# Kernel optimization log

Hardware: AMD Instinct MI355X
Metric: run time of the kernel (lower is better)

Reference implementation:

```python
import jax, jax.numpy as jnp
import numpy as np

B, C, F, NCLS, NWAY = 512, 1024, 14, 100, 64


def setup_inputs() -> dict:
    key = jax.random.key(0)
    k1, k2, k3 = jax.random.split(key, 3)
    query_features = jax.random.normal(k1, (B, C, F, F), dtype=jnp.float32)
    labels = jax.random.randint(k2, (B,), 0, NWAY)
    prototypes = jax.random.normal(k3, (NCLS, C), dtype=jnp.float32) * 0.05
    indices = jnp.arange(NWAY)  # inverse class mapping: episode class i -> global row
    return {"query_features": query_features, "labels": labels,
            "prototypes": prototypes, "indices": indices, "n_way": NWAY}


def reference(query_features, labels, prototypes, indices, n_way):
    b, c, h, w = query_features.shape
    fsq = h * w
    protos = prototypes[indices]                      # [n_way, C]
    # [B,C,H,W] -> [B*H*W, C], matching permute(0,2,3,1).reshape
    q = jnp.transpose(query_features, (0, 2, 3, 1)).reshape(-1, c)
    # -||q - p||^2 via GEMM trick (same math as expanded pairwise diff)
    qn = jnp.sum(q * q, axis=1, keepdims=True)        # [N,1]
    pn = jnp.sum(protos * protos, axis=1)             # [n_way]
    logits = -(qn + pn[None, :] - 2.0 * (q @ protos.T))  # [N, n_way]
    expanded_labels = jnp.repeat(labels, fsq)         # each pixel inherits image label
    logp = jax.nn.log_softmax(logits, axis=1)
    loss = -jnp.mean(jnp.take_along_axis(logp, expanded_labels[:, None], axis=1))
    return loss
```

## Files before the change

kernel.cpp:

```cpp
#include <hip/hip_runtime.h>
#include <hip/hip_bf16.h>

#define C_DIM 1024
#define HW    196
#define NWAY  64
#define HALF_M 98
#define M_PAD 112
#define MT    7
#define BK    64
#define LDK   72
#define N_TOT (512 * 196)

typedef short bf16x8 __attribute__((ext_vector_type(8)));
typedef float floatx4 __attribute__((ext_vector_type(4)));

__device__ __forceinline__ unsigned short f2bf(float x) {
    unsigned int u = __float_as_uint(x);
    u += 0x7fffu + ((u >> 16) & 1u);
    return (unsigned short)(u >> 16);
}

__device__ __forceinline__ bf16x8 pack8(const float v[8]) {
    bf16x8 r;
#pragma unroll
    for (int i = 0; i < 8; ++i) r[i] = (short)f2bf(v[i]);
    return r;
}

__global__ __launch_bounds__(256) void dfmn_main(
    const float* __restrict__ qf, const int* __restrict__ labels,
    const float* __restrict__ protos, const int* __restrict__ indices,
    float* __restrict__ out)
{
    __shared__ __align__(16) float smem[6370];
    __shared__ float pn_lds[NWAY];
    __shared__ float wsum[4];

    const int t    = threadIdx.x;
    const int lane = t & 63;
    const int wave = t >> 6;

    const int x    = blockIdx.x;
    const int xcd  = x & 7;
    const int grp  = x >> 3;
    const int half = grp & 1;
    const int b    = (grp >> 1) * 8 + xcd;
    const int hw0  = half * HALF_M;

    unsigned short* a_lds = (unsigned short*)smem;
    unsigned short* b_lds = a_lds + M_PAD * LDK;
    float* logits = smem;

    {
        const int cls = t >> 2, part = t & 3;
        const int gid = indices[cls];
        const float4* prow = (const float4*)(protos + (size_t)gid * C_DIM) + part * 64;
        float s = 0.f;
#pragma unroll 4
        for (int i = 0; i < 64; ++i) {
            float4 v = prow[i];
            s += v.x * v.x + v.y * v.y + v.z * v.z + v.w * v.w;
        }
        smem[t] = s;
    }
    __syncthreads();
    if (t < NWAY) pn_lds[t] = smem[4 * t] + smem[4 * t + 1] + smem[4 * t + 2] + smem[4 * t + 3];
    __syncthreads();

    const int boct = t & 7;
    const int bcls = t >> 3;
    const float* bsrc0 = protos + (size_t)indices[bcls] * C_DIM + boct * 8;
    const float* bsrc1 = protos + (size_t)indices[bcls + 32] * C_DIM + boct * 8;

    const size_t img_off = (size_t)b * (C_DIM * HW);

    floatx4 acc[MT];
#pragma unroll
    for (int i = 0; i < MT; ++i) acc[i] = (floatx4)0.f;

    const int frm  = lane & 15;
    const int quad = lane >> 4;
    const unsigned short* bfrag_base = b_lds + (wave * 16 + frm) * LDK + quad * 8;

    for (int k0 = 0; k0 < C_DIM; k0 += BK) {
#pragma unroll
        for (int it = 0; it < 4; ++it) {
            int idx = it * 256 + t;
            if (idx < M_PAD * 8) {
                int lr  = idx % M_PAD;
                int oct = idx / M_PAD;
                float v[8];
                if (lr < HALF_M) {
                    const float* src = qf + img_off + (size_t)(k0 + oct * 8) * HW + hw0 + lr;
#pragma unroll
                    for (int j = 0; j < 8; ++j) v[j] = src[(size_t)j * HW];
                } else {
#pragma unroll
                    for (int j = 0; j < 8; ++j) v[j] = 0.f;
                }
                *(bf16x8*)(a_lds + lr * LDK + oct * 8) = pack8(v);
            }
        }
        {
            float4 x0 = *(const float4*)(bsrc0 + k0);
            float4 x1 = *(const float4*)(bsrc0 + k0 + 4);
            float v[8] = {x0.x, x0.y, x0.z, x0.w, x1.x, x1.y, x1.z, x1.w};
            *(bf16x8*)(b_lds + bcls * LDK + boct * 8) = pack8(v);
            float4 y0 = *(const float4*)(bsrc1 + k0);
            float4 y1 = *(const float4*)(bsrc1 + k0 + 4);
            float w[8] = {y0.x, y0.y, y0.z, y0.w, y1.x, y1.y, y1.z, y1.w};
            *(bf16x8*)(b_lds + (bcls + 32) * LDK + boct * 8) = pack8(w);
        }
        __syncthreads();
#pragma unroll
        for (int kk = 0; kk < 2; ++kk) {
            bf16x8 bv = *(const bf16x8*)(bfrag_base + kk * 32);
#pragma unroll
            for (int mt = 0; mt < MT; ++mt) {
                bf16x8 av = *(const bf16x8*)(a_lds + (mt * 16 + frm) * LDK + quad * 8 + kk * 32);
                acc[mt] = __builtin_amdgcn_mfma_f32_16x16x32_bf16(av, bv, acc[mt], 0, 0, 0);
            }
        }
        __syncthreads();
    }

    {
        const int colg = wave * 16 + frm;
        const float pnc = pn_lds[colg];
#pragma unroll
        for (int mt = 0; mt < MT; ++mt) {
#pragma unroll
            for (int r = 0; r < 4; ++r) {
                int row = mt * 16 + quad * 4 + r;
                if (row < HALF_M) logits[row * 65 + colg] = 2.0f * acc[mt][r] - pnc;
            }
        }
    }
    __syncthreads();

    float partial = 0.f;
    if (t < HALF_M) {
        const float* srow = logits + t * 65;
        float mx = -1e30f;
#pragma unroll 8
        for (int c = 0; c < NWAY; ++c) mx = fmaxf(mx, srow[c]);
        float sum = 0.f;
#pragma unroll 8
        for (int c = 0; c < NWAY; ++c) sum += __expf(srow[c] - mx);
        const float lse = mx + __logf(sum);
        partial = (lse - srow[labels[b]]) * (1.0f / (float)N_TOT);
    }
#pragma unroll
    for (int off = 32; off > 0; off >>= 1) partial += __shfl_down(partial, off, 64);
    if (lane == 0) wsum[wave] = partial;
    __syncthreads();
    if (t == 0) atomicAdd(out, wsum[0] + wsum[1] + wsum[2] + wsum[3]);
}

extern "C" void kernel_launch(void* const* d_in, const int* in_sizes, int n_in,
                              void* d_out, int out_size, void* d_ws, size_t ws_size,
                              hipStream_t stream) {
    const float* qf      = (const float*)d_in[0];
    const int*   labels  = (const int*)d_in[1];
    const float* protos  = (const float*)d_in[2];
    const int*   indices = (const int*)d_in[3];

    hipMemsetAsync(d_out, 0, sizeof(float), stream);
    hipLaunchKernelGGL(dfmn_main, dim3(1024), dim3(256), 0, stream,
                       qf, labels, protos, indices, (float*)d_out);
}
```

Baseline: 573.9 us.

## Load full-image fp32 tiles via direct global-to-LDS and fuse softmax in registers

Each block now processes one whole image instead of half. Each K-slab of fp32 query features is copied straight into LDS with global_load_lds, replacing the strided per-thread gathers and the bf16 packing stores. Conversion to bf16 moves to fragment-read time, and each wave handles several M-tiles across all 64 classes. The log-softmax is done in registers with cross-lane shuffles, removing the LDS logits round trip. The cost is a larger LDS footprint with no double buffering, fewer blocks in the grid, and strided LDS reads for the A fragments.

```diff
diff --git a/kernel.cpp b/kernel.cpp
--- a/kernel.cpp
+++ b/kernel.cpp
@@ -4,18 +4,17 @@
 #define C_DIM 1024
 #define HW    196
 #define NWAY  64
-#define HALF_M 98
-#define M_PAD 112
-#define MT    7
 #define BK    64
-#define LDK   72
+#define KSTEPS (C_DIM / BK)
+#define LDB   72
 #define N_TOT (512 * 196)
 
 typedef short bf16x8 __attribute__((ext_vector_type(8)));
 typedef float floatx4 __attribute__((ext_vector_type(4)));
+typedef unsigned int u32;
 
 __device__ __forceinline__ unsigned short f2bf(float x) {
-    unsigned int u = __float_as_uint(x);
+    u32 u = __float_as_uint(x);
     u += 0x7fffu + ((u >> 16) & 1u);
     return (unsigned short)(u >> 16);
 }
@@ -27,129 +26,144 @@
     return r;
 }
 
-__global__ __launch_bounds__(256) void dfmn_main(
+__device__ __forceinline__ void gload16(const float* g, float* l) {
+    __builtin_amdgcn_global_load_lds(
+        (const __attribute__((address_space(1))) u32*)g,
+        (__attribute__((address_space(3))) u32*)l, 16, 0, 0);
+}
+
+__global__ __launch_bounds__(256, 2) void dfmn_main(
     const float* __restrict__ qf, const int* __restrict__ labels,
     const float* __restrict__ protos, const int* __restrict__ indices,
     float* __restrict__ out)
 {
-    __shared__ __align__(16) float smem[6370];
+    __shared__ __align__(16) float a_lds[BK * HW];
+    __shared__ __align__(16) unsigned short b_lds[NWAY * LDB];
     __shared__ float pn_lds[NWAY];
     __shared__ float wsum[4];
 
     const int t    = threadIdx.x;
     const int lane = t & 63;
     const int wave = t >> 6;
-
-    const int x    = blockIdx.x;
-    const int xcd  = x & 7;
-    const int grp  = x >> 3;
-    const int half = grp & 1;
-    const int b    = (grp >> 1) * 8 + xcd;
-    const int hw0  = half * HALF_M;
-
-    unsigned short* a_lds = (unsigned short*)smem;
-    unsigned short* b_lds = a_lds + M_PAD * LDK;
-    float* logits = smem;
+    const int frm  = lane & 15;
+    const int q    = lane >> 4;
+    const int b    = blockIdx.x;
 
     {
         const int cls = t >> 2, part = t & 3;
-        const int gid = indices[cls];
-        const float4* prow = (const float4*)(protos + (size_t)gid * C_DIM) + part * 64;
+        const float* prow = protos + (size_t)indices[cls] * C_DIM + part * 256;
         float s = 0.f;
 #pragma unroll 4
         for (int i = 0; i < 64; ++i) {
-            float4 v = prow[i];
+            float4 v = ((const float4*)prow)[i];
             s += v.x * v.x + v.y * v.y + v.z * v.z + v.w * v.w;
         }
-        smem[t] = s;
+        a_lds[t] = s;
     }
     __syncthreads();
-    if (t < NWAY) pn_lds[t] = smem[4 * t] + smem[4 * t + 1] + smem[4 * t + 2] + smem[4 * t + 3];
+    if (t < NWAY) pn_lds[t] = a_lds[4*t] + a_lds[4*t+1] + a_lds[4*t+2] + a_lds[4*t+3];
     __syncthreads();
 
-    const int boct = t & 7;
-    const int bcls = t >> 3;
-    const float* bsrc0 = protos + (size_t)indices[bcls] * C_DIM + boct * 8;
-    const float* bsrc1 = protos + (size_t)indices[bcls + 32] * C_DIM + boct * 8;
+    const int soct = t & 7;
+    const float* pb0 = protos + (size_t)indices[t >> 3] * C_DIM + soct * 8;
+    const float* pb1 = protos + (size_t)indices[(t + 256) >> 3] * C_DIM + soct * 8;
+    unsigned short* bw0 = &b_lds[(t >> 3) * LDB + soct * 8];
+    unsigned short* bw1 = &b_lds[((t + 256) >> 3) * LDB + soct * 8];
 
-    const size_t img_off = (size_t)b * (C_DIM * HW);
+    const float* qf_img = qf + (size_t)b * (C_DIM * HW);
 
-    floatx4 acc[MT];
+    const int mbase = (wave == 0) ? 0 : 4 + 3 * (wave - 1);
+    const int mcnt  = (wave == 0) ? 4 : 3;
+
+    floatx4 acc[4][4];
 #pragma unroll
-    for (int i = 0; i < MT; ++i) acc[i] = (floatx4)0.f;
+    for (int i = 0; i < 4; ++i)
+#pragma unroll
+        for (int n = 0; n < 4; ++n) acc[i][n] = (floatx4)0.f;
 
-    const int frm  = lane & 15;
-    const int quad = lane >> 4;
-    const unsigned short* bfrag_base = b_lds + (wave * 16 + frm) * LDK + quad * 8;
+    for (int ks = 0; ks < KSTEPS; ++ks) {
+        const int k0 = ks * BK;
+        const float* tile = qf_img + (size_t)k0 * HW;
 
-    for (int k0 = 0; k0 < C_DIM; k0 += BK) {
-#pragma unroll
-        for (int it = 0; it < 4; ++it) {
-            int idx = it * 256 + t;
-            if (idx < M_PAD * 8) {
-                int lr  = idx % M_PAD;
-                int oct = idx / M_PAD;
-                float v[8];
-                if (lr < HALF_M) {
-                    const float* src = qf + img_off + (size_t)(k0 + oct * 8) * HW + hw0 + lr;
-#pragma unroll
-                    for (int j = 0; j < 8; ++j) v[j] = src[(size_t)j * HW];
-                } else {
-#pragma unroll
-                    for (int j = 0; j < 8; ++j) v[j] = 0.f;
-                }
-                *(bf16x8*)(a_lds + lr * LDK + oct * 8) = pack8(v);
-            }
-        }
+        for (int c = wave; c < 49; c += 4)
+            gload16(tile + c * 256 + lane * 4, a_lds + c * 256);
+
         {
-            float4 x0 = *(const float4*)(bsrc0 + k0);
-            float4 x1 = *(const float4*)(bsrc0 + k0 + 4);
+            float4 x0 = *(const float4*)(pb0 + k0);
+            float4 x1 = *(const float4*)(pb0 + k0 + 4);
             float v[8] = {x0.x, x0.y, x0.z, x0.w, x1.x, x1.y, x1.z, x1.w};
-            *(bf16x8*)(b_lds + bcls * LDK + boct * 8) = pack8(v);
-            float4 y0 = *(const float4*)(bsrc1 + k0);
-            float4 y1 = *(const float4*)(bsrc1 + k0 + 4);
+            *(bf16x8*)bw0 = pack8(v);
+            float4 y0 = *(const float4*)(pb1 + k0);
+            float4 y1 = *(const float4*)(pb1 + k0 + 4);
             float w[8] = {y0.x, y0.y, y0.z, y0.w, y1.x, y1.y, y1.z, y1.w};
-            *(bf16x8*)(b_lds + (bcls + 32) * LDK + boct * 8) = pack8(w);
+            *(bf16x8*)bw1 = pack8(w);
         }
         __syncthreads();
+
 #pragma unroll
         for (int kk = 0; kk < 2; ++kk) {
-            bf16x8 bv = *(const bf16x8*)(bfrag_base + kk * 32);
+            const unsigned short* bb = &b_lds[frm * LDB + kk * 32 + q * 8];
+            bf16x8 bv0 = *(const bf16x8*)(bb + 0 * 16 * LDB);
+            bf16x8 bv1 = *(const bf16x8*)(bb + 1 * 16 * LDB);
+            bf16x8 bv2 = *(const bf16x8*)(bb + 2 * 16 * LDB);
+            bf16x8 bv3 = *(const bf16x8*)(bb + 3 * 16 * LDB);
+            const float* ak = a_lds + (kk * 32 + q * 8) * HW + frm;
 #pragma unroll
-            for (int mt = 0; mt < MT; ++mt) {
-                bf16x8 av = *(const bf16x8*)(a_lds + (mt * 16 + frm) * LDK + quad * 8 + kk * 32);
-                acc[mt] = __builtin_amdgcn_mfma_f32_16x16x32_bf16(av, bv, acc[mt], 0, 0, 0);
+            for (int i = 0; i < 4; ++i) {
+                if (i < mcnt) {
+                    const float* ap = ak + (mbase + i) * 16;
+                    float av[8];
+#pragma unroll
+                    for (int j = 0; j < 8; ++j) av[j] = ap[(size_t)j * HW];
+                    bf16x8 a8 = pack8(av);
+                    acc[i][0] = __builtin_amdgcn_mfma_f32_16x16x32_bf16(a8, bv0, acc[i][0], 0, 0, 0);
+                    acc[i][1] = __builtin_amdgcn_mfma_f32_16x16x32_bf16(a8, bv1, acc[i][1], 0, 0, 0);
+                    acc[i][2] = __builtin_amdgcn_mfma_f32_16x16x32_bf16(a8, bv2, acc[i][2], 0, 0, 0);
+                    acc[i][3] = __builtin_amdgcn_mfma_f32_16x16x32_bf16(a8, bv3, acc[i][3], 0, 0, 0);
+                }
             }
         }
         __syncthreads();
     }
 
-    {
-        const int colg = wave * 16 + frm;
-        const float pnc = pn_lds[colg];
+    float pnr[4];
 #pragma unroll
-        for (int mt = 0; mt < MT; ++mt) {
+    for (int n = 0; n < 4; ++n) pnr[n] = pn_lds[n * 16 + frm];
+    const int L   = labels[b];
+    const int ntL = L >> 4;
+    const int fL  = L & 15;
+
+    float partial = 0.f;
+#pragma unroll
+    for (int i = 0; i < 4; ++i) {
+        if (i < mcnt) {
+            const int mt = mbase + i;
 #pragma unroll
             for (int r = 0; r < 4; ++r) {
-                int row = mt * 16 + quad * 4 + r;
-                if (row < HALF_M) logits[row * 65 + colg] = 2.0f * acc[mt][r] - pnc;
+                float l0 = 2.f * acc[i][0][r] - pnr[0];
+                float l1 = 2.f * acc[i][1][r] - pnr[1];
+                float l2 = 2.f * acc[i][2][r] - pnr[2];
+                float l3 = 2.f * acc[i][3][r] - pnr[3];
+                float mx = fmaxf(fmaxf(l0, l1), fmaxf(l2, l3));
+                mx = fmaxf(mx, __shfl_xor(mx, 1));
+                mx = fmaxf(mx, __shfl_xor(mx, 2));
+                mx = fmaxf(mx, __shfl_xor(mx, 4));
+                mx = fmaxf(mx, __shfl_xor(mx, 8));
+                float s = __expf(l0 - mx) + __expf(l1 - mx) + __expf(l2 - mx) + __expf(l3 - mx);
+                s += __shfl_xor(s, 1);
+                s += __shfl_xor(s, 2);
+                s += __shfl_xor(s, 4);
+                s += __shfl_xor(s, 8);
+                float lse = mx + __logf(s);
+                float lL = (ntL == 0) ? l0 : (ntL == 1) ? l1 : (ntL == 2) ? l2 : l3;
+                lL = __shfl(lL, (lane & 48) + fL);
+                const int px = mt * 16 + q * 4 + r;
+                if (px < HW) partial += (lse - lL);
             }
         }
     }
-    __syncthreads();
+    partial *= (1.f / 16.f) * (1.f / (float)N_TOT);
 
-    float partial = 0.f;
-    if (t < HALF_M) {
-        const float* srow = logits + t * 65;
-        float mx = -1e30f;
-#pragma unroll 8
-        for (int c = 0; c < NWAY; ++c) mx = fmaxf(mx, srow[c]);
-        float sum = 0.f;
-#pragma unroll 8
-        for (int c = 0; c < NWAY; ++c) sum += __expf(srow[c] - mx);
-        const float lse = mx + __logf(sum);
-        partial = (lse - srow[labels[b]]) * (1.0f / (float)N_TOT);
-    }
 #pragma unroll
     for (int off = 32; off > 0; off >>= 1) partial += __shfl_down(partial, off, 64);
     if (lane == 0) wsum[wave] = partial;
@@ -166,6 +180,6 @@
     const int*   indices = (const int*)d_in[3];
 
     hipMemsetAsync(d_out, 0, sizeof(float), stream);
-    hipLaunchKernelGGL(dfmn_main, dim3(1024), dim3(256), 0, stream,
+    hipLaunchKernelGGL(dfmn_main, dim3(512), dim3(256), 0, stream,
                        qf, labels, protos, indices, (float*)d_out);
 }
```

New measurement: 559.7 us. 1.03x faster.
